# Performance work log

Hardware: AMD Instinct MI355X
Metric: run time of the kernel (lower is better)

## Reference

```python
import math
import jax, jax.numpy as jnp
import numpy as np

B, C, H, W = 8, 512, 32, 32
NUM_HEADS = 8
HEAD_DIM = C // NUM_HEADS


def setup_inputs() -> dict:
    key = jax.random.key(0)
    ks = jax.random.split(key, 5)
    scale = 1.0 / math.sqrt(C)
    return {
        "x": jax.random.normal(ks[0], (B, C, H, W), dtype=jnp.float32),
        "Wq": jax.random.normal(ks[1], (C, C), dtype=jnp.float32) * scale,
        "bq": jnp.zeros((C,), dtype=jnp.float32),
        "Wk": jax.random.normal(ks[2], (C, C), dtype=jnp.float32) * scale,
        "bk": jnp.zeros((C,), dtype=jnp.float32),
        "Wv": jax.random.normal(ks[3], (C, C), dtype=jnp.float32) * scale,
        "bv": jnp.zeros((C,), dtype=jnp.float32),
        "Wo": jax.random.normal(ks[4], (C, C), dtype=jnp.float32) * scale,
        "bo": jnp.zeros((C,), dtype=jnp.float32),
    }


def reference(x, Wq, bq, Wk, bk, Wv, bv, Wo, bo):
    b, c, h, w = x.shape
    t = h * w
    # (B,C,H,W) -> (B,T,C) token sequence
    xt = x.reshape(b, c, t).transpose(0, 2, 1)
    Q = xt @ Wq + bq
    K = xt @ Wk + bk
    V = xt @ Wv + bv
    # (B,T,C) -> (B,nh,T,hd)
    def split_heads(z):
        return z.reshape(b, t, NUM_HEADS, HEAD_DIM).transpose(0, 2, 1, 3)
    Qh, Kh, Vh = split_heads(Q), split_heads(K), split_heads(V)
    S = jnp.einsum("bhqd,bhkd->bhqk", Qh, Kh) / math.sqrt(HEAD_DIM)
    A = jax.nn.softmax(S, axis=-1)  # dropout p=0.0 -> identity
    Y = jnp.einsum("bhqk,bhkd->bhqd", A, Vh)
    Y = Y.transpose(0, 2, 1, 3).reshape(b, t, c)
    O = Y @ Wo + bo
    out = xt + O
    return out.transpose(0, 2, 1).reshape(b, c, h, w)
```

## Files before the change

### kernel.cpp

```cpp
#include <hip/hip_runtime.h>
#include <hip/hip_bf16.h>

#define B_  8
#define C_  512
#define T_  1024
#define NH_ 8
#define HD_ 64

#define QSCALE 0.1803368801111243f

using short8 = __attribute__((ext_vector_type(8))) short;
using f32x4  = __attribute__((ext_vector_type(4))) float;
using f32x16 = __attribute__((ext_vector_type(16))) float;
using us4    = __attribute__((ext_vector_type(4))) unsigned short;

__device__ __forceinline__ unsigned short f2bf(float f) {
    unsigned u = __builtin_bit_cast(unsigned, f);
    u += 0x7fff + ((u >> 16) & 1);
    return (unsigned short)(u >> 16);
}
__device__ __forceinline__ unsigned pack2bf(float lo, float hi) {
    __hip_bfloat162 h = __float22bfloat162_rn(float2{lo, hi});
    unsigned u;
    __builtin_memcpy(&u, &h, 4);
    return u;
}

__device__ __forceinline__ void gload_lds16(const ushort* g, ushort* l) {
    __builtin_amdgcn_global_load_lds(
        (const __attribute__((address_space(1))) void*)g,
        (__attribute__((address_space(3))) void*)l, 16, 0, 0);
}

template <int N>
__device__ __forceinline__ void wait_vmcnt() {
    asm volatile("s_waitcnt vmcnt(%0)" ::"n"(N) : "memory");
    __builtin_amdgcn_sched_barrier(0);
}
__device__ __forceinline__ void barrier_raw() {
    __builtin_amdgcn_sched_barrier(0);
    __builtin_amdgcn_s_barrier();
}

__global__ __launch_bounds__(256) void k_prep(const float* __restrict__ x,
                                              const float* __restrict__ Wq,
                                              const float* __restrict__ Wk,
                                              const float* __restrict__ Wv,
                                              const float* __restrict__ Wo,
                                              ushort* __restrict__ xt,
                                              ushort* __restrict__ Wqkvt,
                                              ushort* __restrict__ Wot) {
    __shared__ float tile[32][33];
    int L = blockIdx.x;
    int tx = threadIdx.x & 31, ty = threadIdx.x >> 5;
    if (L < 4096) {
        int b = L >> 9, rem = L & 511;
        int t0 = (rem & 31) * 32, c0 = (rem >> 5) * 32;
#pragma unroll
        for (int i = 0; i < 4; i++)
            tile[ty + i * 8][tx] = x[((size_t)b * C_ + c0 + ty + i * 8) * T_ + t0 + tx];
        __syncthreads();
#pragma unroll
        for (int i = 0; i < 4; i++)
            xt[((size_t)b * T_ + t0 + ty + i * 8) * C_ + c0 + tx] = f2bf(tile[tx][ty + i * 8]);
    } else {
        int LL = L - 4096;
        int m = LL >> 8, rem = LL & 255;
        int k0 = (rem & 15) * 32, n0 = (rem >> 4) * 32;
        const float* W = (m == 0) ? Wq : (m == 1) ? Wk : (m == 2) ? Wv : Wo;
        ushort* dst = (m < 3) ? (Wqkvt + (size_t)m * C_ * C_) : Wot;
        float scale = (m == 0) ? QSCALE : 1.0f;
#pragma unroll
        for (int i = 0; i < 4; i++)
            tile[ty + i * 8][tx] = W[(size_t)(k0 + ty + i * 8) * C_ + n0 + tx];
        __syncthreads();
#pragma unroll
        for (int i = 0; i < 4; i++)
            dst[(size_t)(n0 + ty + i * 8) * C_ + k0 + tx] = f2bf(tile[tx][ty + i * 8] * scale);
    }
}

__device__ __forceinline__ void gemm_core(const ushort* __restrict__ A,
                                          const ushort* __restrict__ Bt,
                                          int row0, int col0, int tid,
                                          ushort (*As)[8192], ushort (*Bs)[8192],
                                          f32x4 acc[4][4]) {
    f32x4 zero = {0.f, 0.f, 0.f, 0.f};
#pragma unroll
    for (int i = 0; i < 4; i++)
#pragma unroll
        for (int j = 0; j < 4; j++) acc[i][j] = zero;
    int lane = tid & 63, w = tid >> 6;
    int ql = lane & 15, g = lane >> 4;
    int wm = (w >> 1) * 64, wn = (w & 1) * 64;
    int srow = lane >> 3;
    int scol8 = (lane & 7) ^ (srow & 7);

#pragma unroll
    for (int i = 0; i < 4; i++) {
        int c = w * 4 + i;
        int r = c * 8 + srow;
        gload_lds16(A + (size_t)(row0 + r) * C_ + scol8 * 8, As[0] + c * 512);
        gload_lds16(Bt + (size_t)(col0 + r) * C_ + scol8 * 8, Bs[0] + c * 512);
    }

#pragma unroll
    for (int kt = 0; kt < 8; kt++) {
        int cur = kt & 1;
        if (kt < 7) {
            int k0 = (kt + 1) * 64;
#pragma unroll
            for (int i = 0; i < 4; i++) {
                int c = w * 4 + i;
                int r = c * 8 + srow;
                gload_lds16(A + (size_t)(row0 + r) * C_ + k0 + scol8 * 8, As[cur ^ 1] + c * 512);
                gload_lds16(Bt + (size_t)(col0 + r) * C_ + k0 + scol8 * 8, Bs[cur ^ 1] + c * 512);
            }
            wait_vmcnt<8>();
        } else {
            wait_vmcnt<0>();
        }
        barrier_raw();
        const ushort* Ac = As[cur];
        const ushort* Bc = Bs[cur];
        __builtin_amdgcn_s_setprio(1);
#pragma unroll
        for (int s = 0; s < 2; s++) {
            short8 a[4], b[4];
            int cs = ((4 * s + g) ^ (ql & 7)) * 8;
#pragma unroll
            for (int mt = 0; mt < 4; mt++)
                a[mt] = *(const short8*)(Ac + (wm + mt * 16 + ql) * 64 + cs);
#pragma unroll
            for (int nt = 0; nt < 4; nt++)
                b[nt] = *(const short8*)(Bc + (wn + nt * 16 + ql) * 64 + cs);
#pragma unroll
            for (int mt = 0; mt < 4; mt++)
#pragma unroll
                for (int nt = 0; nt < 4; nt++)
                    acc[mt][nt] = __builtin_amdgcn_mfma_f32_16x16x32_bf16(
                        a[mt], b[nt], acc[mt][nt], 0, 0, 0);
        }
        __builtin_amdgcn_s_setprio(0);
        barrier_raw();
    }
}

__global__ __launch_bounds__(256) void k_qkv(const ushort* __restrict__ xt,
                                             const ushort* __restrict__ Wqkvt,
                                             const float* __restrict__ bq,
                                             const float* __restrict__ bk,
                                             const float* __restrict__ bv,
                                             ushort* __restrict__ Qh,
                                             ushort* __restrict__ Kh,
                                             ushort* __restrict__ Vt) {
    __shared__ __align__(16) ushort As[2][8192];
    __shared__ __align__(16) ushort Bs[2][8192];
    f32x4 acc[4][4];
    int tid = threadIdx.x;
    int L = blockIdx.x;
    int n = L >> 3, xcd = L & 7;
    int row0 = (xcd * 8 + (n & 7)) * 128;
    int col0 = (n >> 3) * 128;
    gemm_core(xt, Wqkvt, row0, col0, tid, As, Bs, acc);
    int lane = tid & 63, w = tid >> 6;
    int ql = lane & 15, g = lane >> 4;
    int wm = (w >> 1) * 64, wn = (w & 1) * 64;
    int which = col0 >> 9;
    const float* bias = (which == 0) ? bq : (which == 1) ? bk : bv;
    float bscale = (which == 0) ? QSCALE : 1.0f;
    ushort* Lt = &As[0][0];

    if (which != 2) {
        ushort* dst = (which == 0) ? Qh : Kh;
#pragma unroll
        for (int mt = 0; mt < 4; mt++)
#pragma unroll
            for (int nt = 0; nt < 4; nt++) {
                int col = wn + nt * 16 + ql;
                float bsv = bias[(col0 + col) & 511] * bscale;
#pragma unroll
                for (int r = 0; r < 4; r++) {
                    int row = wm + mt * 16 + 4 * g + r;
                    int sw = col ^ ((row & 7) << 3);
                    Lt[row * 128 + sw] = f2bf(acc[mt][nt][r] + bsv);
                }
            }
        __syncthreads();
#pragma unroll
        for (int i = 0; i < 8; i++) {
            int task = w * 512 + i * 64 + lane;
            int row = task >> 4, gran = task & 15;
            int sg = gran ^ (row & 7);
            short8 vle = *(const short8*)(Lt + row * 128 + sg * 8);
            int gcol = col0 + gran * 8;
            int hc = gcol & 511, h = hc >> 6, d = hc & 63;
            int grow = row0 + row, b = grow >> 10, t = grow & 1023;
            *(short8*)(dst + ((size_t)(b * NH_ + h) * T_ + t) * HD_ + d) = vle;
        }
    } else {
#pragma unroll
        for (int mt = 0; mt < 4; mt++)
#pragma unroll
            for (int nt = 0; nt < 4; nt++) {
                int col = wn + nt * 16 + ql;
                float bsv = bias[(col0 + col) & 511] * bscale;
                int rowb = wm + mt * 16 + 4 * g;
                int swz = (rowb >> 2) ^ (col & 31);
                us4 pk;
#pragma unroll
                for (int r = 0; r < 4; r++) pk[r] = f2bf(acc[mt][nt][r] + bsv);
                *(us4*)(Lt + col * 128 + swz * 4) = pk;
            }
        __syncthreads();
#pragma unroll
        for (int i = 0; i < 8; i++) {
            int task = w * 512 + i * 64 + lane;
            int colr = task >> 4, gran = task & 15;
            int g4a = (2 * gran) ^ (colr & 31);
            int g4b = (2 * gran + 1) ^ (colr & 31);
            us4 lo = *(const us4*)(Lt + colr * 128 + g4a * 4);
            us4 hi4 = *(const us4*)(Lt + colr * 128 + g4b * 4);
            us4 arr[2] = {lo, hi4};
            short8 vle;
            __builtin_memcpy(&vle, arr, 16);
            int gcol = col0 + colr;
            int hc = gcol & 511, h = hc >> 6, d = hc & 63;
            int grow = row0 + gran * 8, b = grow >> 10, t = grow & 1023;
            *(short8*)(Vt + ((size_t)(b * NH_ + h) * HD_ + d) * T_ + t) = vle;
        }
    }
}

__global__ __launch_bounds__(256) void k_attn(const ushort* __restrict__ Qh,
                                              const ushort* __restrict__ Kh,
                                              const ushort* __restrict__ Vt,
                                              ushort* __restrict__ Y) {
    __shared__ __align__(16) ushort KV[8][4096];
    int tid = threadIdx.x, lane = tid & 63, w = tid >> 6;
    int hi = lane >> 5, l31 = lane & 31, l7 = lane & 7;
    int bh = blockIdx.x & 63, q0 = (blockIdx.x >> 6) * 128;
    int b = bh >> 3, h = bh & 7;
    int srow = lane >> 3;
    int scol8 = l7 ^ (srow & 7);
    const ushort* Kbase = Kh + (size_t)bh * T_ * HD_;
    const ushort* Vbase = Vt + (size_t)bh * HD_ * T_;
    const ushort* kv = &KV[0][0];

    short8 qa[4];
#pragma unroll
    for (int s = 0; s < 4; s++)
        qa[s] = *(const short8*)(Qh + ((size_t)bh * T_ + q0 + w * 32 + l31) * HD_ +
                                 s * 16 + hi * 8);

    int fofs[4];
#pragma unroll
    for (int s = 0; s < 4; s++) fofs[s] = ((2 * s + hi) ^ l7) * 8;
    int rowlo = l31 * 64;

    short8 ones;
    {
        short ov = (l31 == 0) ? (short)0x3F80 : (short)0;
#pragma unroll
        for (int j = 0; j < 8; j++) ones[j] = ov;
    }

    f32x16 o0, o1, o5, z16;
#pragma unroll
    for (int i = 0; i < 16; i++) { o0[i] = 0.f; o1[i] = 0.f; o5[i] = 0.f; z16[i] = 0.f; }

#pragma unroll
    for (int tt = 0; tt < 2; tt++) {
#pragma unroll
        for (int i = 0; i < 2; i++) {
            int c = w * 2 + i;
            int r = c * 8 + srow;
            gload_lds16(Kbase + (size_t)(tt * 64 + r) * HD_ + scol8 * 8,
                        &KV[tt][0] + c * 512);
            gload_lds16(Vbase + (size_t)r * T_ + tt * 64 + scol8 * 8,
                        &KV[4 + tt][0] + c * 512);
        }
    }

#pragma unroll
    for (int t = 0; t < 16; t++) {
        const int sl = t & 3;
        if (t < 14) {
            const int ds = (t + 2) & 3;
            int kv0 = (t + 2) * 64;
#pragma unroll
            for (int i = 0; i < 2; i++) {
                int c = w * 2 + i;
                int r = c * 8 + srow;
                gload_lds16(Kbase + (size_t)(kv0 + r) * HD_ + scol8 * 8,
                            &KV[ds][0] + c * 512);
                gload_lds16(Vbase + (size_t)r * T_ + kv0 + scol8 * 8,
                            &KV[4 + ds][0] + c * 512);
            }
            wait_vmcnt<8>();
        } else if (t == 14) {
            wait_vmcnt<4>();
        } else {
            wait_vmcnt<0>();
        }
        barrier_raw();

        f32x16 sT0, sT1;
        __builtin_amdgcn_s_setprio(1);
        {
            short8 ka0 = *(const short8*)(kv + sl * 4096 + rowlo + fofs[0]);
            short8 ka1 = *(const short8*)(kv + sl * 4096 + 2048 + rowlo + fofs[0]);
            sT0 = __builtin_amdgcn_mfma_f32_32x32x16_bf16(ka0, qa[0], z16, 0, 0, 0);
            sT1 = __builtin_amdgcn_mfma_f32_32x32x16_bf16(ka1, qa[0], z16, 0, 0, 0);
        }
#pragma unroll
        for (int s = 1; s < 4; s++) {
            short8 ka0 = *(const short8*)(kv + sl * 4096 + rowlo + fofs[s]);
            short8 ka1 = *(const short8*)(kv + sl * 4096 + 2048 + rowlo + fofs[s]);
            sT0 = __builtin_amdgcn_mfma_f32_32x32x16_bf16(ka0, qa[s], sT0, 0, 0, 0);
            sT1 = __builtin_amdgcn_mfma_f32_32x32x16_bf16(ka1, qa[s], sT1, 0, 0, 0);
        }
        __builtin_amdgcn_s_setprio(0);

        unsigned pkv0[8], pkv1[8];
#pragma unroll
        for (int i = 0; i < 8; i++) {
            pkv0[i] = pack2bf(__builtin_amdgcn_exp2f(sT0[2 * i]),
                              __builtin_amdgcn_exp2f(sT0[2 * i + 1]));
            pkv1[i] = pack2bf(__builtin_amdgcn_exp2f(sT1[2 * i]),
                              __builtin_amdgcn_exp2f(sT1[2 * i + 1]));
        }

        __builtin_amdgcn_s_setprio(1);
#pragma unroll
        for (int t4 = 0; t4 < 4; t4++) {
            const int h2 = t4 & 1;
            unsigned c0, c1, c2v, c3v;
            if (t4 < 2) {
                c0 = pkv0[4 * h2 + 0]; c2v = pkv0[4 * h2 + 2];
                c1 = pkv0[4 * h2 + 1]; c3v = pkv0[4 * h2 + 3];
            } else {
                c0 = pkv1[4 * h2 + 0]; c2v = pkv1[4 * h2 + 2];
                c1 = pkv1[4 * h2 + 1]; c3v = pkv1[4 * h2 + 3];
            }
            asm("v_permlane32_swap_b32 %0, %1" : "+v"(c0), "+v"(c2v));
            asm("v_permlane32_swap_b32 %0, %1" : "+v"(c1), "+v"(c3v));
            unsigned au[4] = {c0, c1, c2v, c3v};
            short8 pa;
            __builtin_memcpy(&pa, au, 16);
            short8 vb0 = *(const short8*)(kv + (4 + sl) * 4096 + rowlo + fofs[t4]);
            short8 vb1 = *(const short8*)(kv + (4 + sl) * 4096 + 2048 + rowlo + fofs[t4]);
            o0 = __builtin_amdgcn_mfma_f32_32x32x16_bf16(pa, vb0, o0, 0, 0, 0);
            o1 = __builtin_amdgcn_mfma_f32_32x32x16_bf16(pa, vb1, o1, 0, 0, 0);
            o5 = __builtin_amdgcn_mfma_f32_32x32x16_bf16(pa, ones, o5, 0, 0, 0);
        }
        __builtin_amdgcn_s_setprio(0);
    }

#pragma unroll
    for (int r = 0; r < 16; r++) {
        float li = 1.0f / __shfl(o5[r], hi * 32);
        int qr = (r & 3) + 8 * (r >> 2) + 4 * hi;
        int trow = q0 + w * 32 + qr;
        size_t base = ((size_t)b * T_ + trow) * C_ + h * HD_;
        Y[base + l31] = f2bf(o0[r] * li);
        Y[base + 32 + l31] = f2bf(o1[r] * li);
    }
}

__global__ __launch_bounds__(256) void k_oproj(const ushort* __restrict__ Y,
                                               const ushort* __restrict__ Wot,
                                               const float* __restrict__ bo,
                                               const float* __restrict__ x,
                                               float* __restrict__ out) {
    __shared__ __align__(16) ushort As[2][8192];
    __shared__ __align__(16) ushort Bs[2][8192];
    f32x4 acc[4][4];
    int tid = threadIdx.x;
    int L = blockIdx.x;
    int n = L >> 3, xcd = L & 7;
    int row0 = (xcd * 8 + (n & 7)) * 128;
    int col0 = (n >> 3) * 128;
    gemm_core(Y, Wot, row0, col0, tid, As, Bs, acc);
    int lane = tid & 63, w = tid >> 6;
    int wm = (w >> 1) * 64, wn = (w & 1) * 64;
#pragma unroll
    for (int mt = 0; mt < 4; mt++) {
        int grow0 = row0 + wm + mt * 16 + ((lane >> 4) << 2);
        int b = grow0 >> 10, t = grow0 & 1023;
#pragma unroll
        for (int nt = 0; nt < 4; nt++) {
            int c = col0 + wn + nt * 16 + (lane & 15);
            float bsv = bo[c];
            size_t off = ((size_t)b * C_ + c) * T_ + t;
            float4 xv = *(const float4*)(x + off);
            float4 ov;
            ov.x = acc[mt][nt][0] + xv.x + bsv;
            ov.y = acc[mt][nt][1] + xv.y + bsv;
            ov.z = acc[mt][nt][2] + xv.z + bsv;
            ov.w = acc[mt][nt][3] + xv.w + bsv;
            *(float4*)(out + off) = ov;
        }
    }
}

extern "C" void kernel_launch(void* const* d_in, const int* in_sizes, int n_in,
                              void* d_out, int out_size, void* d_ws, size_t ws_size,
                              hipStream_t stream) {
    const float* x  = (const float*)d_in[0];
    const float* Wq = (const float*)d_in[1];
    const float* bq = (const float*)d_in[2];
    const float* Wk = (const float*)d_in[3];
    const float* bk = (const float*)d_in[4];
    const float* Wv = (const float*)d_in[5];
    const float* bv = (const float*)d_in[6];
    const float* Wo = (const float*)d_in[7];
    const float* bo = (const float*)d_in[8];
    float* out = (float*)d_out;

    char* ws = (char*)d_ws;
    ushort* xt    = (ushort*)(ws + 0);
    ushort* Wqkvt = (ushort*)(ws + 8388608);
    ushort* Wot   = (ushort*)(ws + 9961472);
    ushort* Qh    = (ushort*)(ws + 10485760);
    ushort* Kh    = (ushort*)(ws + 18874368);
    ushort* Vt    = (ushort*)(ws + 27262976);
    ushort* Yw    = xt;

    k_prep<<<dim3(5120), 256, 0, stream>>>(x, Wq, Wk, Wv, Wo, xt, Wqkvt, Wot);
    k_qkv<<<dim3(768), 256, 0, stream>>>(xt, Wqkvt, bq, bk, bv, Qh, Kh, Vt);
    k_attn<<<dim3(512), 256, 0, stream>>>(Qh, Kh, Vt, Yw);
    k_oproj<<<dim3(256), 256, 0, stream>>>(Yw, Wot, bo, x, out);
}
```

Measured before the change: 73.26 us.

## Process two 32-row query tiles per wave in attention to reuse K/V fragments

Each wave in the attention kernel now handles 64 query rows instead of 32, reusing every K and V LDS fragment for two query sub-tiles. The grid is halved to 256 blocks with 256 queries per block. This cuts LDS reads and global K/V traffic per query. The cost is much higher register pressure from doubled accumulators, and fewer blocks (256 across roughly 256 CUs), which lowers occupancy and latency hiding. The launch_bounds annotation was also dropped.

```diff
diff --git a/kernel.cpp b/kernel.cpp
--- a/kernel.cpp
+++ b/kernel.cpp
@@ -232,14 +232,14 @@
     }
 }
 
-__global__ __launch_bounds__(256) void k_attn(const ushort* __restrict__ Qh,
-                                              const ushort* __restrict__ Kh,
-                                              const ushort* __restrict__ Vt,
-                                              ushort* __restrict__ Y) {
+__global__ void k_attn(const ushort* __restrict__ Qh,
+                       const ushort* __restrict__ Kh,
+                       const ushort* __restrict__ Vt,
+                       ushort* __restrict__ Y) {
     __shared__ __align__(16) ushort KV[8][4096];
     int tid = threadIdx.x, lane = tid & 63, w = tid >> 6;
     int hi = lane >> 5, l31 = lane & 31, l7 = lane & 7;
-    int bh = blockIdx.x & 63, q0 = (blockIdx.x >> 6) * 128;
+    int bh = blockIdx.x & 63, q0 = (blockIdx.x >> 6) * 256;
     int b = bh >> 3, h = bh & 7;
     int srow = lane >> 3;
     int scol8 = l7 ^ (srow & 7);
@@ -247,11 +247,13 @@
     const ushort* Vbase = Vt + (size_t)bh * HD_ * T_;
     const ushort* kv = &KV[0][0];
 
-    short8 qa[4];
-#pragma unroll
-    for (int s = 0; s < 4; s++)
-        qa[s] = *(const short8*)(Qh + ((size_t)bh * T_ + q0 + w * 32 + l31) * HD_ +
-                                 s * 16 + hi * 8);
+    short8 qaA[4], qaB[4];
+#pragma unroll
+    for (int s = 0; s < 4; s++) {
+        size_t rbase = (size_t)bh * T_ + q0 + w * 64 + l31;
+        qaA[s] = *(const short8*)(Qh + rbase * HD_ + s * 16 + hi * 8);
+        qaB[s] = *(const short8*)(Qh + (rbase + 32) * HD_ + s * 16 + hi * 8);
+    }
 
     int fofs[4];
 #pragma unroll
@@ -265,9 +267,12 @@
         for (int j = 0; j < 8; j++) ones[j] = ov;
     }
 
-    f32x16 o0, o1, o5, z16;
-#pragma unroll
-    for (int i = 0; i < 16; i++) { o0[i] = 0.f; o1[i] = 0.f; o5[i] = 0.f; z16[i] = 0.f; }
+    f32x16 o0a, o1a, o0b, o1b, o5a, o5b, z16;
+#pragma unroll
+    for (int i = 0; i < 16; i++) {
+        o0a[i] = 0.f; o1a[i] = 0.f; o0b[i] = 0.f; o1b[i] = 0.f;
+        o5a[i] = 0.f; o5b[i] = 0.f; z16[i] = 0.f;
+    }
 
 #pragma unroll
     for (int tt = 0; tt < 2; tt++) {
@@ -305,66 +310,89 @@
         }
         barrier_raw();
 
-        f32x16 sT0, sT1;
+        f32x16 sTa0, sTa1, sTb0, sTb1;
         __builtin_amdgcn_s_setprio(1);
         {
             short8 ka0 = *(const short8*)(kv + sl * 4096 + rowlo + fofs[0]);
             short8 ka1 = *(const short8*)(kv + sl * 4096 + 2048 + rowlo + fofs[0]);
-            sT0 = __builtin_amdgcn_mfma_f32_32x32x16_bf16(ka0, qa[0], z16, 0, 0, 0);
-            sT1 = __builtin_amdgcn_mfma_f32_32x32x16_bf16(ka1, qa[0], z16, 0, 0, 0);
+            sTa0 = __builtin_amdgcn_mfma_f32_32x32x16_bf16(ka0, qaA[0], z16, 0, 0, 0);
+            sTa1 = __builtin_amdgcn_mfma_f32_32x32x16_bf16(ka1, qaA[0], z16, 0, 0, 0);
+            sTb0 = __builtin_amdgcn_mfma_f32_32x32x16_bf16(ka0, qaB[0], z16, 0, 0, 0);
+            sTb1 = __builtin_amdgcn_mfma_f32_32x32x16_bf16(ka1, qaB[0], z16, 0, 0, 0);
         }
 #pragma unroll
         for (int s = 1; s < 4; s++) {
             short8 ka0 = *(const short8*)(kv + sl * 4096 + rowlo + fofs[s]);
             short8 ka1 = *(const short8*)(kv + sl * 4096 + 2048 + rowlo + fofs[s]);
-            sT0 = __builtin_amdgcn_mfma_f32_32x32x16_bf16(ka0, qa[s], sT0, 0, 0, 0);
-            sT1 = __builtin_amdgcn_mfma_f32_32x32x16_bf16(ka1, qa[s], sT1, 0, 0, 0);
+            sTa0 = __builtin_amdgcn_mfma_f32_32x32x16_bf16(ka0, qaA[s], sTa0, 0, 0, 0);
+            sTa1 = __builtin_amdgcn_mfma_f32_32x32x16_bf16(ka1, qaA[s], sTa1, 0, 0, 0);
+            sTb0 = __builtin_amdgcn_mfma_f32_32x32x16_bf16(ka0, qaB[s], sTb0, 0, 0, 0);
+            sTb1 = __builtin_amdgcn_mfma_f32_32x32x16_bf16(ka1, qaB[s], sTb1, 0, 0, 0);
         }
         __builtin_amdgcn_s_setprio(0);
 
-        unsigned pkv0[8], pkv1[8];
+        unsigned pkva0[8], pkva1[8], pkvb0[8], pkvb1[8];
 #pragma unroll
         for (int i = 0; i < 8; i++) {
-            pkv0[i] = pack2bf(__builtin_amdgcn_exp2f(sT0[2 * i]),
-                              __builtin_amdgcn_exp2f(sT0[2 * i + 1]));
-            pkv1[i] = pack2bf(__builtin_amdgcn_exp2f(sT1[2 * i]),
-                              __builtin_amdgcn_exp2f(sT1[2 * i + 1]));
+            pkva0[i] = pack2bf(__builtin_amdgcn_exp2f(sTa0[2 * i]),
+                               __builtin_amdgcn_exp2f(sTa0[2 * i + 1]));
+            pkva1[i] = pack2bf(__builtin_amdgcn_exp2f(sTa1[2 * i]),
+                               __builtin_amdgcn_exp2f(sTa1[2 * i + 1]));
+            pkvb0[i] = pack2bf(__builtin_amdgcn_exp2f(sTb0[2 * i]),
+                               __builtin_amdgcn_exp2f(sTb0[2 * i + 1]));
+            pkvb1[i] = pack2bf(__builtin_amdgcn_exp2f(sTb1[2 * i]),
+                               __builtin_amdgcn_exp2f(sTb1[2 * i + 1]));
         }
 
         __builtin_amdgcn_s_setprio(1);
 #pragma unroll
         for (int t4 = 0; t4 < 4; t4++) {
             const int h2 = t4 & 1;
-            unsigned c0, c1, c2v, c3v;
+            unsigned a0, a1, a2, a3, b0, b1, b2, b3;
             if (t4 < 2) {
-                c0 = pkv0[4 * h2 + 0]; c2v = pkv0[4 * h2 + 2];
-                c1 = pkv0[4 * h2 + 1]; c3v = pkv0[4 * h2 + 3];
+                a0 = pkva0[4 * h2 + 0]; a2 = pkva0[4 * h2 + 2];
+                a1 = pkva0[4 * h2 + 1]; a3 = pkva0[4 * h2 + 3];
+                b0 = pkvb0[4 * h2 + 0]; b2 = pkvb0[4 * h2 + 2];
+                b1 = pkvb0[4 * h2 + 1]; b3 = pkvb0[4 * h2 + 3];
             } else {
-                c0 = pkv1[4 * h2 + 0]; c2v = pkv1[4 * h2 + 2];
-                c1 = pkv1[4 * h2 + 1]; c3v = pkv1[4 * h2 + 3];
+                a0 = pkva1[4 * h2 + 0]; a2 = pkva1[4 * h2 + 2];
+                a1 = pkva1[4 * h2 + 1]; a3 = pkva1[4 * h2 + 3];
+                b0 = pkvb1[4 * h2 + 0]; b2 = pkvb1[4 * h2 + 2];
+                b1 = pkvb1[4 * h2 + 1]; b3 = pkvb1[4 * h2 + 3];
             }
-            asm("v_permlane32_swap_b32 %0, %1" : "+v"(c0), "+v"(c2v));
-            asm("v_permlane32_swap_b32 %0, %1" : "+v"(c1), "+v"(c3v));
-            unsigned au[4] = {c0, c1, c2v, c3v};
-            short8 pa;
-            __builtin_memcpy(&pa, au, 16);
+            asm("v_permlane32_swap_b32 %0, %1" : "+v"(a0), "+v"(a2));
+            asm("v_permlane32_swap_b32 %0, %1" : "+v"(a1), "+v"(a3));
+            asm("v_permlane32_swap_b32 %0, %1" : "+v"(b0), "+v"(b2));
+            asm("v_permlane32_swap_b32 %0, %1" : "+v"(b1), "+v"(b3));
+            unsigned auA[4] = {a0, a1, a2, a3};
+            unsigned auB[4] = {b0, b1, b2, b3};
+            short8 paA, paB;
+            __builtin_memcpy(&paA, auA, 16);
+            __builtin_memcpy(&paB, auB, 16);
             short8 vb0 = *(const short8*)(kv + (4 + sl) * 4096 + rowlo + fofs[t4]);
             short8 vb1 = *(const short8*)(kv + (4 + sl) * 4096 + 2048 + rowlo + fofs[t4]);
-            o0 = __builtin_amdgcn_mfma_f32_32x32x16_bf16(pa, vb0, o0, 0, 0, 0);
-            o1 = __builtin_amdgcn_mfma_f32_32x32x16_bf16(pa, vb1, o1, 0, 0, 0);
-            o5 = __builtin_amdgcn_mfma_f32_32x32x16_bf16(pa, ones, o5, 0, 0, 0);
+            o0a = __builtin_amdgcn_mfma_f32_32x32x16_bf16(paA, vb0, o0a, 0, 0, 0);
+            o1a = __builtin_amdgcn_mfma_f32_32x32x16_bf16(paA, vb1, o1a, 0, 0, 0);
+            o0b = __builtin_amdgcn_mfma_f32_32x32x16_bf16(paB, vb0, o0b, 0, 0, 0);
+            o1b = __builtin_amdgcn_mfma_f32_32x32x16_bf16(paB, vb1, o1b, 0, 0, 0);
+            o5a = __builtin_amdgcn_mfma_f32_32x32x16_bf16(paA, ones, o5a, 0, 0, 0);
+            o5b = __builtin_amdgcn_mfma_f32_32x32x16_bf16(paB, ones, o5b, 0, 0, 0);
         }
         __builtin_amdgcn_s_setprio(0);
     }
 
 #pragma unroll
     for (int r = 0; r < 16; r++) {
-        float li = 1.0f / __shfl(o5[r], hi * 32);
         int qr = (r & 3) + 8 * (r >> 2) + 4 * hi;
-        int trow = q0 + w * 32 + qr;
-        size_t base = ((size_t)b * T_ + trow) * C_ + h * HD_;
-        Y[base + l31] = f2bf(o0[r] * li);
-        Y[base + 32 + l31] = f2bf(o1[r] * li);
+        float liA = 1.0f / __shfl(o5a[r], hi * 32);
+        float liB = 1.0f / __shfl(o5b[r], hi * 32);
+        int trowA = q0 + w * 64 + qr;
+        size_t baseA = ((size_t)b * T_ + trowA) * C_ + h * HD_;
+        Y[baseA + l31] = f2bf(o0a[r] * liA);
+        Y[baseA + 32 + l31] = f2bf(o1a[r] * liA);
+        size_t baseB = baseA + (size_t)32 * C_;
+        Y[baseB + l31] = f2bf(o0b[r] * liB);
+        Y[baseB + 32 + l31] = f2bf(o1b[r] * liB);
     }
 }
 
@@ -429,6 +457,6 @@
 
     k_prep<<<dim3(5120), 256, 0, stream>>>(x, Wq, Wk, Wv, Wo, xt, Wqkvt, Wot);
     k_qkv<<<dim3(768), 256, 0, stream>>>(xt, Wqkvt, bq, bk, bv, Qh, Kh, Vt);
-    k_attn<<<dim3(512), 256, 0, stream>>>(Qh, Kh, Vt, Yw);
+    k_attn<<<dim3(256), 256, 0, stream>>>(Qh, Kh, Vt, Yw);
     k_oproj<<<dim3(256), 256, 0, stream>>>(Yw, Wot, bo, x, out);
 }
```

Result: slower. 261.5 us (+256.9%).

## Software-pipeline attention loop: overlap PV of previous tile with exp of current

Applied to the files above, without the earlier changes.

Restructures the flash-attention inner loop so the PV MFMAs for tile t-1 run after the QK^T MFMAs for tile t, while the exp/pack of tile t's scores is held in double-buffered registers. The intent is to let the transcendental exp work overlap with matrix-core work instead of serialising them. The wait/barrier is also moved before issuing the next prefetch, which changes the in-flight load depth. This raises register pressure from the doubled P buffers and relies on the 4-slot LDS ring keeping tile t-1's V valid while the tile t+2 prefetch is issued.

```diff
diff --git a/kernel.cpp b/kernel.cpp
--- a/kernel.cpp
+++ b/kernel.cpp
@@ -269,6 +269,31 @@
 #pragma unroll
     for (int i = 0; i < 16; i++) { o0[i] = 0.f; o1[i] = 0.f; o5[i] = 0.f; z16[i] = 0.f; }
 
+    unsigned pk0[2][8], pk1[2][8];
+
+#define PV_BLOCK(P0, P1, VSL)                                                   \
+    __builtin_amdgcn_s_setprio(1);                                              \
+    _Pragma("unroll")                                                           \
+    for (int t4 = 0; t4 < 4; t4++) {                                            \
+        const int h2 = t4 & 1;                                                  \
+        unsigned c0, c1, c2v, c3v;                                              \
+        if (t4 < 2) { c0 = (P0)[4 * h2 + 0]; c2v = (P0)[4 * h2 + 2];            \
+                      c1 = (P0)[4 * h2 + 1]; c3v = (P0)[4 * h2 + 3]; }          \
+        else        { c0 = (P1)[4 * h2 + 0]; c2v = (P1)[4 * h2 + 2];            \
+                      c1 = (P1)[4 * h2 + 1]; c3v = (P1)[4 * h2 + 3]; }          \
+        asm("v_permlane32_swap_b32 %0, %1" : "+v"(c0), "+v"(c2v));              \
+        asm("v_permlane32_swap_b32 %0, %1" : "+v"(c1), "+v"(c3v));              \
+        unsigned au[4] = {c0, c1, c2v, c3v};                                    \
+        short8 pa;                                                              \
+        __builtin_memcpy(&pa, au, 16);                                          \
+        short8 vb0 = *(const short8*)(kv + (4 + (VSL)) * 4096 + rowlo + fofs[t4]);        \
+        short8 vb1 = *(const short8*)(kv + (4 + (VSL)) * 4096 + 2048 + rowlo + fofs[t4]); \
+        o0 = __builtin_amdgcn_mfma_f32_32x32x16_bf16(pa, vb0, o0, 0, 0, 0);     \
+        o1 = __builtin_amdgcn_mfma_f32_32x32x16_bf16(pa, vb1, o1, 0, 0, 0);     \
+        o5 = __builtin_amdgcn_mfma_f32_32x32x16_bf16(pa, ones, o5, 0, 0, 0);    \
+    }                                                                           \
+    __builtin_amdgcn_s_setprio(0);
+
 #pragma unroll
     for (int tt = 0; tt < 2; tt++) {
 #pragma unroll
@@ -285,6 +310,13 @@
 #pragma unroll
     for (int t = 0; t < 16; t++) {
         const int sl = t & 3;
+        const int par = t & 1;
+        if (t < 15) {
+            wait_vmcnt<4>();
+        } else {
+            wait_vmcnt<0>();
+        }
+        barrier_raw();
         if (t < 14) {
             const int ds = (t + 2) & 3;
             int kv0 = (t + 2) * 64;
@@ -297,13 +329,7 @@
                 gload_lds16(Vbase + (size_t)r * T_ + kv0 + scol8 * 8,
                             &KV[4 + ds][0] + c * 512);
             }
-            wait_vmcnt<8>();
-        } else if (t == 14) {
-            wait_vmcnt<4>();
-        } else {
-            wait_vmcnt<0>();
-        }
-        barrier_raw();
+        }
 
         f32x16 sT0, sT1;
         __builtin_amdgcn_s_setprio(1);
@@ -322,40 +348,23 @@
         }
         __builtin_amdgcn_s_setprio(0);
 
-        unsigned pkv0[8], pkv1[8];
+        if (t == 1 || t == 3 || t == 5 || t == 7 || t == 9 || t == 11 || t == 13 || t == 15) {
+            PV_BLOCK(pk0[0], pk1[0], (t - 1) & 3)
+        } else if (t > 0) {
+            PV_BLOCK(pk0[1], pk1[1], (t - 1) & 3)
+        }
+
 #pragma unroll
         for (int i = 0; i < 8; i++) {
-            pkv0[i] = pack2bf(__builtin_amdgcn_exp2f(sT0[2 * i]),
-                              __builtin_amdgcn_exp2f(sT0[2 * i + 1]));
-            pkv1[i] = pack2bf(__builtin_amdgcn_exp2f(sT1[2 * i]),
-                              __builtin_amdgcn_exp2f(sT1[2 * i + 1]));
-        }
-
-        __builtin_amdgcn_s_setprio(1);
-#pragma unroll
-        for (int t4 = 0; t4 < 4; t4++) {
-            const int h2 = t4 & 1;
-            unsigned c0, c1, c2v, c3v;
-            if (t4 < 2) {
-                c0 = pkv0[4 * h2 + 0]; c2v = pkv0[4 * h2 + 2];
-                c1 = pkv0[4 * h2 + 1]; c3v = pkv0[4 * h2 + 3];
-            } else {
-                c0 = pkv1[4 * h2 + 0]; c2v = pkv1[4 * h2 + 2];
-                c1 = pkv1[4 * h2 + 1]; c3v = pkv1[4 * h2 + 3];
-            }
-            asm("v_permlane32_swap_b32 %0, %1" : "+v"(c0), "+v"(c2v));
-            asm("v_permlane32_swap_b32 %0, %1" : "+v"(c1), "+v"(c3v));
-            unsigned au[4] = {c0, c1, c2v, c3v};
-            short8 pa;
-            __builtin_memcpy(&pa, au, 16);
-            short8 vb0 = *(const short8*)(kv + (4 + sl) * 4096 + rowlo + fofs[t4]);
-            short8 vb1 = *(const short8*)(kv + (4 + sl) * 4096 + 2048 + rowlo + fofs[t4]);
-            o0 = __builtin_amdgcn_mfma_f32_32x32x16_bf16(pa, vb0, o0, 0, 0, 0);
-            o1 = __builtin_amdgcn_mfma_f32_32x32x16_bf16(pa, vb1, o1, 0, 0, 0);
-            o5 = __builtin_amdgcn_mfma_f32_32x32x16_bf16(pa, ones, o5, 0, 0, 0);
-        }
-        __builtin_amdgcn_s_setprio(0);
-    }
+            pk0[par][i] = pack2bf(__builtin_amdgcn_exp2f(sT0[2 * i]),
+                                  __builtin_amdgcn_exp2f(sT0[2 * i + 1]));
+            pk1[par][i] = pack2bf(__builtin_amdgcn_exp2f(sT1[2 * i]),
+                                  __builtin_amdgcn_exp2f(sT1[2 * i + 1]));
+        }
+    }
+
+    PV_BLOCK(pk0[1], pk1[1], 3)
+#undef PV_BLOCK
 
 #pragma unroll
     for (int r = 0; r < 16; r++) {
```

New measurement: 72.46 us, median of 2. About the same (-1.1%).
